# Performance work log

Hardware: AMD Instinct MI355X
Metric: run time of the kernel (lower is better)

The kernel has to match this reference:

```python
import jax, jax.numpy as jnp
import numpy as np

EMBED_DIM = 512
NUM_HEADS = 8
HEAD_DIM = EMBED_DIM // NUM_HEADS
SCALE = HEAD_DIM ** -0.5
B, N = 4, 2048


def _linear_params(key, fan_in, fan_out):
    kw, kb = jax.random.split(key)
    bound = 1.0 / np.sqrt(fan_in)
    W = jax.random.uniform(kw, (fan_out, fan_in), minval=-bound, maxval=bound, dtype=jnp.float32)
    b = jax.random.uniform(kb, (fan_out,), minval=-bound, maxval=bound, dtype=jnp.float32)
    return W, b


def setup_inputs() -> dict:
    key = jax.random.key(0)
    ks = jax.random.split(key, 7)
    query = jax.random.normal(ks[0], (B, N, EMBED_DIM), dtype=jnp.float32)
    k_in = jax.random.normal(ks[1], (B, N, EMBED_DIM), dtype=jnp.float32)
    v_in = jax.random.normal(ks[2], (B, N, EMBED_DIM), dtype=jnp.float32)
    Wq, bq = _linear_params(ks[3], EMBED_DIM, EMBED_DIM)
    Wk, bk = _linear_params(ks[4], EMBED_DIM, EMBED_DIM)
    Wv, bv = _linear_params(ks[5], EMBED_DIM, EMBED_DIM)
    Wo, bo = _linear_params(ks[6], EMBED_DIM, EMBED_DIM)
    return {
        "query": query, "key": k_in, "value": v_in,
        "Wq": Wq, "bq": bq, "Wk": Wk, "bk": bk,
        "Wv": Wv, "bv": bv, "Wo": Wo, "bo": bo,
    }


def reference(query, key, value, Wq, bq, Wk, bk, Wv, bv, Wo, bo):
    Bq, Nq, _ = query.shape
    # projections: (B, S, E) x (E, E)^T + b
    q = (query @ Wq.T + bq).reshape(Bq, Nq, NUM_HEADS, HEAD_DIM).transpose(0, 2, 1, 3)  # bhnd
    k = (key @ Wk.T + bk).reshape(Bq, -1, NUM_HEADS, HEAD_DIM).transpose(0, 2, 1, 3)    # bhmd
    v = (value @ Wv.T + bv).reshape(Bq, -1, NUM_HEADS, HEAD_DIM).transpose(0, 2, 1, 3)  # bhmd
    attn = jnp.einsum('bhnd,bhmd->bhnm', q, k) * SCALE
    attn = jax.nn.softmax(attn, axis=-1)
    x = jnp.einsum('bhnm,bhmd->bhnd', attn, v)
    x = x.transpose(0, 2, 1, 3).reshape(Bq, Nq, EMBED_DIM)
    return x @ Wo.T + bo
```

## Files before the change

kernel.cpp:

```cpp
#include <hip/hip_runtime.h>
#include <stdint.h>

#define NX (8192*512)
#define NW (512*512)

typedef __bf16 bf16x8 __attribute__((ext_vector_type(8)));
typedef float  f32x4  __attribute__((ext_vector_type(4)));
typedef float  f32x16 __attribute__((ext_vector_type(16)));

__device__ __forceinline__ unsigned short f2bf(float f){
  unsigned u = __builtin_bit_cast(unsigned, f);
  u += 0x7FFFu + ((u >> 16) & 1u);
  return (unsigned short)(u >> 16);
}

__device__ __forceinline__ f32x4 mfma16(bf16x8 a, bf16x8 b, f32x4 c){
  return __builtin_amdgcn_mfma_f32_16x16x32_bf16(a, b, c, 0, 0, 0);
}
__device__ __forceinline__ f32x16 mfma32(bf16x8 a, bf16x8 b, f32x16 c){
  return __builtin_amdgcn_mfma_f32_32x32x16_bf16(a, b, c, 0, 0, 0);
}

__device__ __forceinline__ void gload_lds16(const void* g, void* l){
  __builtin_amdgcn_global_load_lds((const __attribute__((address_space(1))) void*)g,
                                   (__attribute__((address_space(3))) void*)l, 16, 0, 0);
}

#define VMCNT(n) asm volatile("s_waitcnt vmcnt(" #n ")" ::: "memory")

__global__ void convert_all(const float* __restrict__ q, const float* __restrict__ k,
                            const float* __restrict__ v, const float* __restrict__ wq,
                            const float* __restrict__ wk, const float* __restrict__ wv,
                            const float* __restrict__ wo, unsigned short* __restrict__ dst)
{
  const long total4 = (3L*NX + 4L*NW) / 4;
  for (long i = (long)blockIdx.x*blockDim.x + threadIdx.x; i < total4; i += (long)gridDim.x*blockDim.x){
    long e = i*4;
    const float* src; long off;
    if (e < NX)            { src = q;  off = e; }
    else if (e < 2L*NX)    { src = k;  off = e - NX; }
    else if (e < 3L*NX)    { src = v;  off = e - 2L*NX; }
    else {
      long w = e - 3L*NX; int wi = (int)(w / NW); off = w - (long)wi*NW;
      src = (wi==0) ? wq : (wi==1) ? wk : (wi==2) ? wv : wo;
    }
    float4 f = *(const float4*)(src + off);
    ushort4 o; o.x=f2bf(f.x); o.y=f2bf(f.y); o.z=f2bf(f.z); o.w=f2bf(f.w);
    *(ushort4*)(dst + e) = o;
  }
}

struct GArg {
  const unsigned short* A;
  const unsigned short* B;
  const float* bias;
  void* C;
  float scale;
  int mode;
};

__global__ __launch_bounds__(256) void gemm_bt(GArg g0, GArg g1, GArg g2)
{
  GArg g = (blockIdx.z==0) ? g0 : (blockIdx.z==1) ? g1 : g2;
  __shared__ __attribute__((aligned(16))) unsigned char lds[65536];
  const int tid  = threadIdx.x;
  const int lane = tid & 63;
  const int wid  = tid >> 6;
  const int wr = wid >> 1, wc = wid & 1;
  const int m0 = blockIdx.y * 128;
  const int n0 = blockIdx.x * 128;

  f32x4 acc[4][4];
  #pragma unroll
  for (int s=0;s<4;s++)
    #pragma unroll
    for (int t=0;t<4;t++) acc[s][t] = (f32x4){0.f,0.f,0.f,0.f};

  auto stage = [&](int kt, int buf){
    int Lb = tid*16;
    #pragma unroll
    for (int i=0;i<4;i++){
      int L = Lb + i*4096;
      int row = L >> 7;
      int innerS = (L & 127) ^ ((row & 7) << 4);
      gload_lds16(g.A + (size_t)(m0+row)*512 + kt*64 + (innerS>>1), lds + buf*16384 + L);
    }
    #pragma unroll
    for (int i=0;i<4;i++){
      int L = Lb + i*4096;
      int row = L >> 7;
      int innerS = (L & 127) ^ ((row & 7) << 4);
      gload_lds16(g.B + (size_t)(n0+row)*512 + kt*64 + (innerS>>1), lds + 32768 + buf*16384 + L);
    }
  };

  stage(0, 0);
  VMCNT(0);
  __syncthreads();

  for (int kt=0; kt<8; kt++){
    int cur = kt & 1;
    if (kt < 7) stage(kt+1, cur^1);
    const unsigned char* LA = lds + cur*16384;
    const unsigned char* LB = lds + 32768 + cur*16384;
    #pragma unroll
    for (int ks=0; ks<2; ks++){
      bf16x8 af[4], bfr[4];
      #pragma unroll
      for (int s=0;s<4;s++){
        int row = wr*64 + s*16 + (lane & 15);
        int inner = (ks*32 + (lane>>4)*8)*2;
        af[s] = *(const bf16x8*)(LA + row*128 + (inner ^ ((row&7)<<4)));
      }
      #pragma unroll
      for (int t=0;t<4;t++){
        int row = wc*64 + t*16 + (lane & 15);
        int inner = (ks*32 + (lane>>4)*8)*2;
        bfr[t] = *(const bf16x8*)(LB + row*128 + (inner ^ ((row&7)<<4)));
      }
      #pragma unroll
      for (int s=0;s<4;s++)
        #pragma unroll
        for (int t=0;t<4;t++)
          acc[s][t] = mfma16(af[s], bfr[t], acc[s][t]);
    }
    VMCNT(0);
    __syncthreads();
  }

  if (g.mode == 2){
    float* C = (float*)g.C;
    #pragma unroll
    for (int t=0;t<4;t++){
      int col = n0 + wc*64 + t*16 + (lane&15);
      float bv = g.bias[col];
      #pragma unroll
      for (int s=0;s<4;s++){
        #pragma unroll
        for (int r=0;r<4;r++){
          int row = m0 + wr*64 + s*16 + (lane>>4)*4 + r;
          C[(size_t)row*512 + col] = acc[s][t][r] + bv;
        }
      }
    }
  } else if (g.mode == 0){
    unsigned short* C = (unsigned short*)g.C;
    #pragma unroll
    for (int t=0;t<4;t++){
      int col = n0 + wc*64 + t*16 + (lane&15);
      float bv = g.bias[col];
      #pragma unroll
      for (int s=0;s<4;s++){
        #pragma unroll
        for (int r=0;r<4;r++){
          int row = m0 + wr*64 + s*16 + (lane>>4)*4 + r;
          C[(size_t)row*512 + col] = f2bf((acc[s][t][r] + bv) * g.scale);
        }
      }
    }
  } else {
    __syncthreads();
    unsigned short* T = (unsigned short*)lds;
    #pragma unroll
    for (int s=0;s<4;s++){
      #pragma unroll
      for (int t=0;t<4;t++){
        int col  = wc*64 + t*16 + (lane&15);
        int rowb = wr*64 + s*16 + (lane>>4)*4;
        float bv = g.bias[n0+col];
        ushort4 pk;
        pk.x = f2bf(acc[s][t][0] + bv);
        pk.y = f2bf(acc[s][t][1] + bv);
        pk.z = f2bf(acc[s][t][2] + bv);
        pk.w = f2bf(acc[s][t][3] + bv);
        *(ushort4*)(T + col*136 + rowb) = pk;
      }
    }
    __syncthreads();
    unsigned short* Vt = (unsigned short*)g.C;
    int col = tid >> 1, half = tid & 1;
    int gcol = n0 + col;
    int hh = gcol >> 6, d = gcol & 63;
    int b = m0 >> 11, ms = m0 & 2047;
    unsigned short* dst = Vt + (((size_t)(b*8+hh)*64 + d)*2048 + ms + half*64);
    const unsigned short* srcT = T + col*136 + half*64;
    #pragma unroll
    for (int j=0;j<8;j++)
      *(int4*)(dst + j*8) = *(const int4*)(srcT + j*8);
  }
}

__global__ __launch_bounds__(256) void attn_kernel(
    const unsigned short* __restrict__ Qs,
    const unsigned short* __restrict__ Kb,
    const unsigned short* __restrict__ Vt,
    unsigned short* __restrict__ AO)
{
  __shared__ __attribute__((aligned(16))) unsigned char lds[22528];
  const int tid = threadIdx.x, lane = tid & 63, wid = tid >> 6;
  const int hi = lane >> 5, lq = lane & 31;

  const int flat = blockIdx.y*16 + blockIdx.x;
  const int work = (flat & 7)*64 + (flat >> 3);
  const int bh = work >> 4, qtile = work & 15;
  const int b = bh >> 3, h = bh & 7;
  const int q0 = qtile*128 + wid*32;

  const unsigned short* Kbase = Kb + (size_t)b*2048*512 + h*64;
  const unsigned short* Vbase = Vt + (size_t)bh*64*2048;
  unsigned char* VLDS = lds + 12288;

  bf16x8 qf[4];
  #pragma unroll
  for (int c=0;c<4;c++)
    qf[c] = *(const bf16x8*)(Qs + (size_t)(b*2048 + q0 + lq)*512 + h*64 + c*16 + hi*8);

  int koff[4], voff[2][2];
  #pragma unroll
  for (int c=0;c<4;c++)
    koff[c] = lq*128 + ((c*32 + hi*16) ^ ((lq & 7) << 4));
  #pragma unroll
  for (int dh=0;dh<2;dh++)
    #pragma unroll
    for (int cb=0;cb<2;cb++)
      voff[dh][cb] = (dh*32 + lq)*80 + cb*32 + hi*16;

  const int sL = tid >> 3;
  const int sI = (tid & 7) * 16;
  const int sArow = (sL&3) + 4*((sL>>3)&1) + 8*((sL>>2)&1) + 16*((sL>>4)&1);
  const int sSrc = ((sI ^ ((sL & 7) << 4)) >> 1);
  const int vrow = tid >> 2, vpart = tid & 3;

  auto stageK = [&](int t, int buf){
    gload_lds16(Kbase + (size_t)(t*32 + sArow)*512 + sSrc, lds + buf*4096 + tid*16);
  };
  auto loadV = [&](int t){
    return *(const uint4*)(Vbase + (size_t)vrow*2048 + t*32 + vpart*8);
  };
  auto writeV = [&](int buf, uint4 v){
    *(uint4*)(VLDS + buf*5120 + vrow*80 + vpart*16) = v;
  };

  f32x16 o[2];
  o[0] = (f32x16)(0.f); o[1] = (f32x16)(0.f);
  float m_run = -1e30f, l_run = 0.f;
  const float LOG2E = 1.44269504f;

  auto compute = [&](const unsigned char* KL, const unsigned char* VL){
    f32x16 S = (f32x16)(0.f);
    #pragma unroll
    for (int c=0;c<4;c++){
      bf16x8 kf = *(const bf16x8*)(KL + koff[c]);
      S = mfma32(kf, qf[c], S);
    }

    float mt = fmaxf(S[0], S[1]);
    #pragma unroll
    for (int r=2;r<16;r++) mt = fmaxf(mt, S[r]);
    mt = fmaxf(mt, __shfl_xor(mt, 32));

    if (!__all(mt <= m_run + 8.0f)){
      float mn = fmaxf(m_run, mt);
      float corr = exp2f((m_run - mn)*LOG2E);
      l_run *= corr;
      m_run = mn;
      #pragma unroll
      for (int r=0;r<16;r++){ o[0][r] *= corr; o[1][r] *= corr; }
    }

    float mc = m_run * LOG2E;
    float p[16];
    #pragma unroll
    for (int r=0;r<16;r++) p[r] = exp2f(S[r]*LOG2E - mc);

    float rs = p[0] + p[1];
    #pragma unroll
    for (int r=2;r<16;r++) rs += p[r];
    rs += __shfl_xor(rs, 32);
    l_run += rs;

    bf16x8 pf0, pf1;
    #pragma unroll
    for (int j=0;j<8;j++){ pf0[j] = (__bf16)p[j]; pf1[j] = (__bf16)p[8+j]; }

    #pragma unroll
    for (int dh=0;dh<2;dh++){
      bf16x8 v0 = *(const bf16x8*)(VL + voff[dh][0]);
      o[dh] = mfma32(v0, pf0, o[dh]);
      bf16x8 v1 = *(const bf16x8*)(VL + voff[dh][1]);
      o[dh] = mfma32(v1, pf1, o[dh]);
    }
  };

  stageK(0, 0); stageK(1, 1);
  uint4 VgA = loadV(0);
  uint4 VgB = loadV(1);
  VMCNT(1);
  writeV(0, VgA);
  __syncthreads();

  for (int t=0; t<62; t+=2){
    stageK(t+2, (t+2)%3); VgA = loadV(t+2);
    compute(lds + (t%3)*4096, VLDS);
    VMCNT(2);
    writeV(1, VgB);
    __syncthreads();
    stageK(t+3, (t+3)%3); VgB = loadV(t+3);
    compute(lds + ((t+1)%3)*4096, VLDS + 5120);
    VMCNT(2);
    writeV(0, VgA);
    __syncthreads();
  }
  compute(lds + 2*4096, VLDS);
  VMCNT(0);
  writeV(1, VgB);
  __syncthreads();
  compute(lds + 0*4096, VLDS + 5120);

  {
    float inv = 1.0f / l_run;
    unsigned short* dst = AO + (size_t)(b*2048 + q0 + lq)*512 + h*64;
    #pragma unroll
    for (int dh=0;dh<2;dh++){
      #pragma unroll
      for (int g2=0;g2<4;g2++){
        ushort4 pk;
        pk.x = f2bf(o[dh][g2*4+0]*inv);
        pk.y = f2bf(o[dh][g2*4+1]*inv);
        pk.z = f2bf(o[dh][g2*4+2]*inv);
        pk.w = f2bf(o[dh][g2*4+3]*inv);
        *(ushort4*)(dst + dh*32 + g2*8 + hi*4) = pk;
      }
    }
  }
}

extern "C" void kernel_launch(void* const* d_in, const int* in_sizes, int n_in,
                              void* d_out, int out_size, void* d_ws, size_t ws_size,
                              hipStream_t stream)
{
  const float* q  = (const float*)d_in[0];
  const float* k  = (const float*)d_in[1];
  const float* v  = (const float*)d_in[2];
  const float* Wq = (const float*)d_in[3];
  const float* bq = (const float*)d_in[4];
  const float* Wk = (const float*)d_in[5];
  const float* bk = (const float*)d_in[6];
  const float* Wv = (const float*)d_in[7];
  const float* bv = (const float*)d_in[8];
  const float* Wo = (const float*)d_in[9];
  const float* bo = (const float*)d_in[10];

  unsigned short* X   = (unsigned short*)d_ws;
  unsigned short* Xq  = X;
  unsigned short* Xk  = X + NX;
  unsigned short* Xv  = X + 2*(size_t)NX;
  unsigned short* WqB = X + 3*(size_t)NX;
  unsigned short* WkB = WqB + NW;
  unsigned short* WvB = WqB + 2*(size_t)NW;
  unsigned short* WoB = WqB + 3*(size_t)NW;
  unsigned short* QS  = WqB + 4*(size_t)NW;
  unsigned short* KB  = QS + NX;
  unsigned short* VT  = KB + NX;
  unsigned short* AO  = VT + NX;

  convert_all<<<dim3(2048), dim3(256), 0, stream>>>(q, k, v, Wq, Wk, Wv, Wo, X);

  GArg gq{Xq, WqB, bq, (void*)QS, 0.125f, 0};
  GArg gk{Xk, WkB, bk, (void*)KB, 1.0f,   0};
  GArg gv{Xv, WvB, bv, (void*)VT, 1.0f,   1};
  gemm_bt<<<dim3(4, 64, 3), dim3(256), 0, stream>>>(gq, gk, gv);

  attn_kernel<<<dim3(16, 32), dim3(256), 0, stream>>>(QS, KB, VT, AO);

  GArg go{AO, WoB, bo, d_out, 1.0f, 2};
  gemm_bt<<<dim3(4, 64, 1), dim3(256), 0, stream>>>(go, go, go);
}
```

Measured before the change: 121.0 us.

## Software-pipeline QK^T one tile ahead and fold log2e into Q scale

Result: no change. 119.1 us (-1.6%).

```diff
diff --git a/kernel.cpp b/kernel.cpp
--- a/kernel.cpp
+++ b/kernel.cpp
@@ -196,7 +196,7 @@
     const unsigned short* __restrict__ Vt,
     unsigned short* __restrict__ AO)
 {
-  __shared__ __attribute__((aligned(16))) unsigned char lds[22528];
+  __shared__ __attribute__((aligned(16))) unsigned char lds[27648];
   const int tid = threadIdx.x, lane = tid & 63, wid = tid >> 6;
   const int hi = lane >> 5, lq = lane & 31;
 
@@ -229,7 +229,8 @@
   const int sI = (tid & 7) * 16;
   const int sArow = (sL&3) + 4*((sL>>3)&1) + 8*((sL>>2)&1) + 16*((sL>>4)&1);
   const int sSrc = ((sI ^ ((sL & 7) << 4)) >> 1);
-  const int vrow = tid >> 2, vpart = tid & 3;
+  const int vrow = wid*16 + (lane & 15);
+  const int vpart = lane >> 4;
 
   auto stageK = [&](int t, int buf){
     gload_lds16(Kbase + (size_t)(t*32 + sArow)*512 + sSrc, lds + buf*4096 + tid*16);
@@ -244,38 +245,41 @@
   f32x16 o[2];
   o[0] = (f32x16)(0.f); o[1] = (f32x16)(0.f);
   float m_run = -1e30f, l_run = 0.f;
-  const float LOG2E = 1.44269504f;
-
-  auto compute = [&](const unsigned char* KL, const unsigned char* VL){
+
+  auto qkt = [&](const unsigned char* KL) -> f32x16 {
     f32x16 S = (f32x16)(0.f);
     #pragma unroll
     for (int c=0;c<4;c++){
       bf16x8 kf = *(const bf16x8*)(KL + koff[c]);
       S = mfma32(kf, qf[c], S);
     }
-
-    float mt = fmaxf(S[0], S[1]);
-    #pragma unroll
-    for (int r=2;r<16;r++) mt = fmaxf(mt, S[r]);
+    return S;
+  };
+
+  auto finish = [&](f32x16 S, const unsigned char* VL){
+    float a0 = fmaxf(fmaxf(S[0],S[1]),S[2]);
+    float a1 = fmaxf(fmaxf(S[3],S[4]),S[5]);
+    float a2 = fmaxf(fmaxf(S[6],S[7]),S[8]);
+    float a3 = fmaxf(fmaxf(S[9],S[10]),S[11]);
+    float a4 = fmaxf(fmaxf(S[12],S[13]),S[14]);
+    float mt = fmaxf(fmaxf(fmaxf(a0,a1),a2), fmaxf(fmaxf(a3,a4),S[15]));
     mt = fmaxf(mt, __shfl_xor(mt, 32));
 
-    if (!__all(mt <= m_run + 8.0f)){
+    if (!__all(mt <= m_run + 11.5415603f)){
       float mn = fmaxf(m_run, mt);
-      float corr = exp2f((m_run - mn)*LOG2E);
+      float corr = exp2f(m_run - mn);
       l_run *= corr;
       m_run = mn;
       #pragma unroll
       for (int r=0;r<16;r++){ o[0][r] *= corr; o[1][r] *= corr; }
     }
 
-    float mc = m_run * LOG2E;
     float p[16];
     #pragma unroll
-    for (int r=0;r<16;r++) p[r] = exp2f(S[r]*LOG2E - mc);
-
-    float rs = p[0] + p[1];
-    #pragma unroll
-    for (int r=2;r<16;r++) rs += p[r];
+    for (int r=0;r<16;r++) p[r] = exp2f(S[r] - m_run);
+
+    float rs = (((p[0]+p[1])+(p[2]+p[3]))+((p[4]+p[5])+(p[6]+p[7])))
+             + (((p[8]+p[9])+(p[10]+p[11]))+((p[12]+p[13])+(p[14]+p[15])));
     rs += __shfl_xor(rs, 32);
     l_run += rs;
 
@@ -294,28 +298,32 @@
 
   stageK(0, 0); stageK(1, 1);
   uint4 VgA = loadV(0);
-  uint4 VgB = loadV(1);
-  VMCNT(1);
-  writeV(0, VgA);
+  VMCNT(0); writeV(0, VgA);
   __syncthreads();
+  VgA = loadV(1); stageK(2, 2);
+  f32x16 S_a = qkt(lds);
+  VMCNT(1); writeV(1, VgA);
+  __syncthreads();
 
   for (int t=0; t<62; t+=2){
-    stageK(t+2, (t+2)%3); VgA = loadV(t+2);
-    compute(lds + (t%3)*4096, VLDS);
-    VMCNT(2);
-    writeV(1, VgB);
-    __syncthreads();
-    stageK(t+3, (t+3)%3); VgB = loadV(t+3);
-    compute(lds + ((t+1)%3)*4096, VLDS + 5120);
-    VMCNT(2);
-    writeV(0, VgA);
-    __syncthreads();
-  }
-  compute(lds + 2*4096, VLDS);
-  VMCNT(0);
-  writeV(1, VgB);
-  __syncthreads();
-  compute(lds + 0*4096, VLDS + 5120);
+    VgA = loadV(t+2);
+    stageK(t+3, t%3);
+    f32x16 S_b = qkt(lds + ((t+1)%3)*4096);
+    finish(S_a, VLDS + (t%3)*5120);
+    VMCNT(1); writeV((t+2)%3, VgA);
+    __syncthreads();
+    VgA = loadV(t+3);
+    if (t < 60) stageK(t+4, (t+1)%3);
+    S_a = qkt(lds + ((t+2)%3)*4096);
+    finish(S_b, VLDS + ((t+1)%3)*5120);
+    VMCNT(1); writeV((t+3)%3, VgA);
+    __syncthreads();
+  }
+  {
+    f32x16 S_b = qkt(lds + 0*4096);
+    finish(S_a, VLDS + 2*5120);
+    finish(S_b, VLDS + 0*5120);
+  }
 
   {
     float inv = 1.0f / l_run;
@@ -366,7 +374,7 @@
 
   convert_all<<<dim3(2048), dim3(256), 0, stream>>>(q, k, v, Wq, Wk, Wv, Wo, X);
 
-  GArg gq{Xq, WqB, bq, (void*)QS, 0.125f, 0};
+  GArg gq{Xq, WqB, bq, (void*)QS, 0.180336878f, 0};
   GArg gk{Xk, WkB, bk, (void*)KB, 1.0f,   0};
   GArg gv{Xv, WvB, bv, (void*)VT, 1.0f,   1};
   gemm_bt<<<dim3(4, 64, 3), dim3(256), 0, stream>>>(gq, gk, gv);
```
